# Performance work log

Hardware: AMD Instinct MI355X
Metric: run time of the kernel (lower is better)

The kernel has to match this reference:

```python
import jax, jax.numpy as jnp
import numpy as np

EPS = 1e-8  # torch.cosine_similarity default eps


def setup_inputs() -> dict:
    key = jax.random.key(0)
    ks = jax.random.split(key, 6)
    B, U, P, H = 256, 128, 64, 768
    utt_output = jax.random.normal(ks[0], (U, B, H), dtype=jnp.float32)
    pheno_output = jax.random.normal(ks[1], (P, B, H), dtype=jnp.float32)
    # Conv1d(in=U, out=U, kernel=P) weight: [out, in, kernel]
    w_utt = jax.random.normal(ks[2], (U, U, P), dtype=jnp.float32) / np.sqrt(U * P)
    b_utt = jax.random.normal(ks[3], (U,), dtype=jnp.float32) * 0.01
    # Conv1d(in=P, out=P, kernel=U) weight: [out, in, kernel]
    w_pheno = jax.random.normal(ks[4], (P, P, U), dtype=jnp.float32) / np.sqrt(P * U)
    b_pheno = jax.random.normal(ks[5], (P,), dtype=jnp.float32) * 0.01
    return {"utt_output": utt_output, "pheno_output": pheno_output,
            "w_utt": w_utt, "b_utt": b_utt, "w_pheno": w_pheno, "b_pheno": b_pheno}


def reference(utt_output, pheno_output, w_utt, b_utt, w_pheno, b_pheno):
    # [len, B, H] -> [B, len, H]
    u = jnp.swapaxes(utt_output, 0, 1)    # [B, U, H]
    p = jnp.swapaxes(pheno_output, 0, 1)  # [B, P, H]
    # cosine similarity matrix c[b,i,j] = <u_i, p_j> / (max(|u_i|,eps)*max(|p_j|,eps))
    un = u / jnp.maximum(jnp.linalg.norm(u, axis=-1, keepdims=True), EPS)
    pn = p / jnp.maximum(jnp.linalg.norm(p, axis=-1, keepdims=True), EPS)
    c = jnp.einsum('buh,bph->bup', un, pn)  # [B, U, P]
    # Conv1d with kernel covering the full width -> output length 1, i.e. an einsum
    row_logits = jnp.einsum('bup,oup->bo', c, w_utt) + b_utt        # [B, U]
    col_logits = jnp.einsum('bup,opu->bo', c, w_pheno) + b_pheno    # [B, P]
    row_attention = jax.nn.softmax(row_logits, axis=-1)
    col_attention = jax.nn.softmax(col_logits, axis=-1)
    return row_attention, col_attention
```

## Files before the change

### kernel.cpp

```cpp
#include <hip/hip_runtime.h>
#include <stdint.h>

#define Bn 256
#define Un 128
#define Pn 64
#define Hn 768
#define Ototal 192
#define KC 16

#define CH 64
#define NCH 12
#define LDU 72
#define LDB 56

typedef short s4v __attribute__((ext_vector_type(4)));
typedef short s8v __attribute__((ext_vector_type(8)));
typedef float f4v __attribute__((ext_vector_type(4)));

__device__ __forceinline__ short f2bf(float x) {
  union { float f; uint32_t u; } c; c.f = x;
  uint32_t r = (c.u + 0x7fffu + ((c.u >> 16) & 1u)) >> 16;
  return (short)(r & 0xffffu);
}

__global__ void __launch_bounds__(256) convW(const float* __restrict__ w_utt,
                                             const float* __restrict__ w_ph,
                                             ushort* __restrict__ Wbf) {
  __shared__ float tile[64 * 129];
  const int bx = blockIdx.x;
  const int t = threadIdx.x;
  if (bx < 4096) {
    int idx = bx * 256 + t;
    Wbf[idx] = (ushort)f2bf(w_utt[idx]);
    return;
  }
  const int oc = bx - 4096;
  const float* src = w_ph + (size_t)oc * 8192;
#pragma unroll
  for (int itr = 0; itr < 8; ++itr) {
    int idx = itr * 1024 + t * 4;
    int j = idx >> 7, i = idx & 127;
    float4 v = *(const float4*)(src + idx);
    tile[j * 129 + i + 0] = v.x;
    tile[j * 129 + i + 1] = v.y;
    tile[j * 129 + i + 2] = v.z;
    tile[j * 129 + i + 3] = v.w;
  }
  __syncthreads();
  const size_t obase = (size_t)(128 + oc) * 8192;
#pragma unroll
  for (int itr = 0; itr < 8; ++itr) {
    int k = itr * 1024 + t * 4;
    int i = k >> 6, j = k & 63;
    s4v o4 = { f2bf(tile[(j + 0) * 129 + i]),
               f2bf(tile[(j + 1) * 129 + i]),
               f2bf(tile[(j + 2) * 129 + i]),
               f2bf(tile[(j + 3) * 129 + i]) };
    *(s4v*)&Wbf[obase + k] = o4;
  }
}

__global__ void __launch_bounds__(1024, 4) phaseA(const float* __restrict__ utt,
                                                  const float* __restrict__ ph,
                                                  ushort* __restrict__ Cbf) {
  const int b = blockIdx.x;
  const int t = threadIdx.x;
  const int w = t >> 6, l = t & 63;

  __shared__ short uA[2][Un * LDU];
  __shared__ short pB[2][Pn * LDU];
  __shared__ float s_inu[Un];
  __shared__ float s_inp[Pn];

  const int ur = t >> 3;
  const int uc = (t & 7) * 8;
  const int pr = t >> 4;
  const int pc = (t & 15) * 4;

  const size_t rstride = (size_t)Bn * Hn;
  const float* ubase = utt + (size_t)b * Hn + (size_t)ur * rstride + uc;
  const float* pbase = ph  + (size_t)b * Hn + (size_t)pr * rstride + pc;

  float4 ru0[2], ru1[2], rp[2];
#pragma unroll
  for (int s = 0; s < 2; ++s) {
    ru0[s] = *(const float4*)(ubase + s * CH);
    ru1[s] = *(const float4*)(ubase + s * CH + 4);
    rp[s]  = *(const float4*)(pbase + s * CH);
  }

  float ssu = 0.f, ssp = 0.f;
  f4v zero4 = {0.f, 0.f, 0.f, 0.f};
  f4v acc[2] = {zero4, zero4};

  const int m  = l & 15;
  const int ko = (l >> 4) * 8;
  const int it = w & 7;
  const int jp = w >> 3;

  const int ua_w = ur * LDU + uc;
  const int pb_w = pr * LDU + pc;

#pragma unroll
  for (int c = 0; c < NCH; ++c) {
    const int s = c & 1;
    float4 a0 = ru0[s], a1 = ru1[s], p0 = rp[s];
    ssu += a0.x*a0.x + a0.y*a0.y + a0.z*a0.z + a0.w*a0.w
         + a1.x*a1.x + a1.y*a1.y + a1.z*a1.z + a1.w*a1.w;
    ssp += p0.x*p0.x + p0.y*p0.y + p0.z*p0.z + p0.w*p0.w;
    if (c + 2 < NCH) {
      ru0[s] = *(const float4*)(ubase + (c + 2) * CH);
      ru1[s] = *(const float4*)(ubase + (c + 2) * CH + 4);
      rp[s]  = *(const float4*)(pbase + (c + 2) * CH);
    }
    s8v au = { f2bf(a0.x), f2bf(a0.y), f2bf(a0.z), f2bf(a0.w),
               f2bf(a1.x), f2bf(a1.y), f2bf(a1.z), f2bf(a1.w) };
    s4v pp = { f2bf(p0.x), f2bf(p0.y), f2bf(p0.z), f2bf(p0.w) };
    *(s8v*)&uA[s][ua_w] = au;
    *(s4v*)&pB[s][pb_w] = pp;
    __syncthreads();
    const short* ab = &uA[s][(it * 16 + m) * LDU + ko];
    const short* bb = &pB[s][(jp * 32 + m) * LDU + ko];
#pragma unroll
    for (int ks = 0; ks < 2; ++ks) {
      s8v af = *(const s8v*)(ab + ks * 32);
#pragma unroll
      for (int jt = 0; jt < 2; ++jt) {
        s8v bf = *(const s8v*)(bb + jt * 16 * LDU + ks * 32);
        acc[jt] = __builtin_amdgcn_mfma_f32_16x16x32_bf16(af, bf, acc[jt], 0, 0, 0);
      }
    }
  }

  ssu += __shfl_xor(ssu, 4); ssu += __shfl_xor(ssu, 2); ssu += __shfl_xor(ssu, 1);
  ssp += __shfl_xor(ssp, 8); ssp += __shfl_xor(ssp, 4);
  ssp += __shfl_xor(ssp, 2); ssp += __shfl_xor(ssp, 1);
  if ((t & 7) == 0)  s_inu[ur] = 1.f / fmaxf(sqrtf(ssu), 1e-8f);
  if ((t & 15) == 0) s_inp[pr] = 1.f / fmaxf(sqrtf(ssp), 1e-8f);
  __syncthreads();

  const int cl = l & 15;
  const int rq = (l >> 4) * 4;
#pragma unroll
  for (int jt = 0; jt < 2; ++jt) {
    int j = jp * 32 + jt * 16 + cl;
    float sj = s_inp[j];
#pragma unroll
    for (int r = 0; r < 4; ++r) {
      int il = it * 16 + rq + r;
      float v = acc[jt][r] * s_inu[il] * sj;
      Cbf[((size_t)b * Un + il) * Pn + j] = (ushort)f2bf(v);
    }
  }
}

__global__ void __launch_bounds__(256) phaseB(const ushort* __restrict__ Cbf,
                                              const ushort* __restrict__ Wbf,
                                              float* __restrict__ partial) {
  const int kc = blockIdx.x;
  const int mt = blockIdx.y;
  const int nt = blockIdx.z;
  const int t = threadIdx.x;
  const int w = t >> 6, l = t & 63;

  __shared__ short Ab[64 * LDB];
  __shared__ short Bb[64 * LDB];

  const int row = t >> 2;
  const int ko8 = (t & 3) * 8;

  f4v zero4 = {0.f, 0.f, 0.f, 0.f};
  f4v acc[4] = {zero4, zero4, zero4, zero4};

  const ushort* Ag = Cbf + (size_t)(mt * 64 + row) * 8192 + kc * 512 + ko8;
  const ushort* Bg = Wbf + (size_t)(nt * 64 + row) * 8192 + kc * 512 + ko8;
  const int m  = l & 15;
  const int ko = (l >> 4) * 8;

  for (int c = 0; c < 16; ++c) {
    s8v av = *(const s8v*)(Ag + c * 32);
    s8v bv = *(const s8v*)(Bg + c * 32);
    __syncthreads();
    *(s8v*)&Ab[row * LDB + ko8] = av;
    *(s8v*)&Bb[row * LDB + ko8] = bv;
    __syncthreads();
    s8v af = *(const s8v*)&Ab[(16 * w + m) * LDB + ko];
#pragma unroll
    for (int jt = 0; jt < 4; ++jt) {
      s8v bf = *(const s8v*)&Bb[(16 * jt + m) * LDB + ko];
      acc[jt] = __builtin_amdgcn_mfma_f32_16x16x32_bf16(af, bf, acc[jt], 0, 0, 0);
    }
  }

  const int rq = (l >> 4) * 4;
#pragma unroll
  for (int jt = 0; jt < 4; ++jt) {
    int og = nt * 64 + 16 * jt + (l & 15);
#pragma unroll
    for (int r = 0; r < 4; ++r) {
      int bg = mt * 64 + 16 * w + rq + r;
      partial[((size_t)kc * Bn + bg) * Ototal + og] = acc[jt][r];
    }
  }
}

__global__ void __launch_bounds__(192) phaseC(const float* __restrict__ partial,
                                              const float* __restrict__ b_utt,
                                              const float* __restrict__ b_ph,
                                              float* __restrict__ out) {
  const int b = blockIdx.x;
  const int t = threadIdx.x;
  const int w = t >> 6, l = t & 63;

  float v = 0.f;
#pragma unroll
  for (int kc = 0; kc < KC; ++kc)
    v += partial[((size_t)kc * Bn + b) * Ototal + t];
  v += (t < Un) ? b_utt[t] : b_ph[t - Un];

  __shared__ float red[3];
  float mx = v;
  for (int o = 32; o >= 1; o >>= 1) mx = fmaxf(mx, __shfl_xor(mx, o));
  if (l == 0) red[w] = mx;
  __syncthreads();
  float gmax = (t < Un) ? fmaxf(red[0], red[1]) : red[2];
  float e = expf(v - gmax);
  float s = e;
  for (int o = 32; o >= 1; o >>= 1) s += __shfl_xor(s, o);
  __syncthreads();
  if (l == 0) red[w] = s;
  __syncthreads();
  float gs = (t < Un) ? (red[0] + red[1]) : red[2];
  float r = e / gs;
  if (t < Un) out[(size_t)b * Un + t] = r;
  else        out[(size_t)Bn * Un + (size_t)b * Pn + (t - Un)] = r;
}

extern "C" void kernel_launch(void* const* d_in, const int* in_sizes, int n_in,
                              void* d_out, int out_size, void* d_ws, size_t ws_size,
                              hipStream_t stream) {
  const float* utt   = (const float*)d_in[0];
  const float* ph    = (const float*)d_in[1];
  const float* w_utt = (const float*)d_in[2];
  const float* b_utt = (const float*)d_in[3];
  const float* w_ph  = (const float*)d_in[4];
  const float* b_ph  = (const float*)d_in[5];

  char* ws = (char*)d_ws;
  ushort* Cbf     = (ushort*)(ws);
  ushort* Wbf     = (ushort*)(ws + 4194304);
  float*  partial = (float*)(ws + 7340032);

  convW <<<dim3(4096 + 64), dim3(256), 0, stream>>>(w_utt, w_ph, Wbf);
  phaseA<<<dim3(Bn), dim3(1024), 0, stream>>>(utt, ph, Cbf);
  phaseB<<<dim3(KC, 4, 3), dim3(256), 0, stream>>>(Cbf, Wbf, partial);
  phaseC<<<dim3(Bn), dim3(192), 0, stream>>>(partial, b_utt, b_ph, (float*)d_out);
}
```

Baseline: 245.7 us.

## Split phaseA per batch into two U-halves and widen phaseB K-step

phaseA now launches two 512-thread blocks per batch, each computing the cosine block for 64 of the 128 utterance rows. The H loop moves to 32-wide chunks with single-buffered shared memory and a one-step register prefetch. The change is meant to raise block count and occupancy and to shrink per-block shared memory, at the cost of the pheno rows being loaded and normalised twice. phaseB now stages 64 K-values per barrier pair instead of 32, which halves its synchronisations and issues two MFMA k-steps per stage.

```diff
diff --git a/kernel.cpp b/kernel.cpp
--- a/kernel.cpp
+++ b/kernel.cpp
@@ -8,10 +8,8 @@
 #define Ototal 192
 #define KC 16
 
-#define CH 64
-#define NCH 12
-#define LDU 72
-#define LDB 56
+#define LDU 40
+#define LDB 72
 
 typedef short s4v __attribute__((ext_vector_type(4)));
 typedef short s8v __attribute__((ext_vector_type(8)));
@@ -60,83 +58,69 @@
   }
 }
 
-__global__ void __launch_bounds__(1024, 4) phaseA(const float* __restrict__ utt,
-                                                  const float* __restrict__ ph,
-                                                  ushort* __restrict__ Cbf) {
-  const int b = blockIdx.x;
+__global__ void __launch_bounds__(512) phaseA(const float* __restrict__ utt,
+                                              const float* __restrict__ ph,
+                                              ushort* __restrict__ Cbf) {
+  const int bx = blockIdx.x;
+  const int b = bx >> 1, half = bx & 1;
   const int t = threadIdx.x;
   const int w = t >> 6, l = t & 63;
 
-  __shared__ short uA[2][Un * LDU];
-  __shared__ short pB[2][Pn * LDU];
-  __shared__ float s_inu[Un];
-  __shared__ float s_inp[Pn];
-
-  const int ur = t >> 3;
-  const int uc = (t & 7) * 8;
-  const int pr = t >> 4;
-  const int pc = (t & 15) * 4;
+  __shared__ short uA[64 * LDU];
+  __shared__ short pB[64 * LDU];
+  __shared__ float s_inu[64];
+  __shared__ float s_inp[64];
+
+  const int r  = t >> 3;
+  const int cc = (t & 7) * 4;
 
   const size_t rstride = (size_t)Bn * Hn;
-  const float* ubase = utt + (size_t)b * Hn + (size_t)ur * rstride + uc;
-  const float* pbase = ph  + (size_t)b * Hn + (size_t)pr * rstride + pc;
-
-  float4 ru0[2], ru1[2], rp[2];
-#pragma unroll
-  for (int s = 0; s < 2; ++s) {
-    ru0[s] = *(const float4*)(ubase + s * CH);
-    ru1[s] = *(const float4*)(ubase + s * CH + 4);
-    rp[s]  = *(const float4*)(pbase + s * CH);
-  }
+  const float* ubase = utt + (size_t)b * Hn + (size_t)(half * 64 + r) * rstride + cc;
+  const float* pbase = ph  + (size_t)b * Hn + (size_t)r * rstride + cc;
+
+  float4 ru = *(const float4*)ubase;
+  float4 rp = *(const float4*)pbase;
 
   float ssu = 0.f, ssp = 0.f;
   f4v zero4 = {0.f, 0.f, 0.f, 0.f};
-  f4v acc[2] = {zero4, zero4};
+  f4v acc0 = zero4, acc1 = zero4;
 
   const int m  = l & 15;
   const int ko = (l >> 4) * 8;
-  const int it = w & 7;
-  const int jp = w >> 3;
-
-  const int ua_w = ur * LDU + uc;
-  const int pb_w = pr * LDU + pc;
-
-#pragma unroll
-  for (int c = 0; c < NCH; ++c) {
-    const int s = c & 1;
-    float4 a0 = ru0[s], a1 = ru1[s], p0 = rp[s];
-    ssu += a0.x*a0.x + a0.y*a0.y + a0.z*a0.z + a0.w*a0.w
-         + a1.x*a1.x + a1.y*a1.y + a1.z*a1.z + a1.w*a1.w;
+  const int it = w & 3;
+  const int jp = w >> 2;
+  const int lw = r * LDU + (t & 7) * 4;
+
+  const short* ab = &uA[(it * 16 + m) * LDU + ko];
+  const short* bb = &pB[(jp * 32 + m) * LDU + ko];
+
+  for (int c = 0; c < 24; ++c) {
+    __syncthreads();
+    float4 a = ru, p0 = rp;
+    ssu += a.x*a.x + a.y*a.y + a.z*a.z + a.w*a.w;
     ssp += p0.x*p0.x + p0.y*p0.y + p0.z*p0.z + p0.w*p0.w;
-    if (c + 2 < NCH) {
-      ru0[s] = *(const float4*)(ubase + (c + 2) * CH);
-      ru1[s] = *(const float4*)(ubase + (c + 2) * CH + 4);
-      rp[s]  = *(const float4*)(pbase + (c + 2) * CH);
-    }
-    s8v au = { f2bf(a0.x), f2bf(a0.y), f2bf(a0.z), f2bf(a0.w),
-               f2bf(a1.x), f2bf(a1.y), f2bf(a1.z), f2bf(a1.w) };
+    s4v au = { f2bf(a.x),  f2bf(a.y),  f2bf(a.z),  f2bf(a.w)  };
     s4v pp = { f2bf(p0.x), f2bf(p0.y), f2bf(p0.z), f2bf(p0.w) };
-    *(s8v*)&uA[s][ua_w] = au;
-    *(s4v*)&pB[s][pb_w] = pp;
-    __syncthreads();
-    const short* ab = &uA[s][(it * 16 + m) * LDU + ko];
-    const short* bb = &pB[s][(jp * 32 + m) * LDU + ko];
-#pragma unroll
-    for (int ks = 0; ks < 2; ++ks) {
-      s8v af = *(const s8v*)(ab + ks * 32);
-#pragma unroll
-      for (int jt = 0; jt < 2; ++jt) {
-        s8v bf = *(const s8v*)(bb + jt * 16 * LDU + ks * 32);
-        acc[jt] = __builtin_amdgcn_mfma_f32_16x16x32_bf16(af, bf, acc[jt], 0, 0, 0);
-      }
-    }
+    *(s4v*)&uA[lw] = au;
+    *(s4v*)&pB[lw] = pp;
+    __syncthreads();
+    if (c < 23) {
+      ru = *(const float4*)(ubase + (c + 1) * 32);
+      rp = *(const float4*)(pbase + (c + 1) * 32);
+    }
+    s8v af  = *(const s8v*)ab;
+    s8v bf0 = *(const s8v*)bb;
+    s8v bf1 = *(const s8v*)(bb + 16 * LDU);
+    acc0 = __builtin_amdgcn_mfma_f32_16x16x32_bf16(af, bf0, acc0, 0, 0, 0);
+    acc1 = __builtin_amdgcn_mfma_f32_16x16x32_bf16(af, bf1, acc1, 0, 0, 0);
   }
 
   ssu += __shfl_xor(ssu, 4); ssu += __shfl_xor(ssu, 2); ssu += __shfl_xor(ssu, 1);
-  ssp += __shfl_xor(ssp, 8); ssp += __shfl_xor(ssp, 4);
-  ssp += __shfl_xor(ssp, 2); ssp += __shfl_xor(ssp, 1);
-  if ((t & 7) == 0)  s_inu[ur] = 1.f / fmaxf(sqrtf(ssu), 1e-8f);
-  if ((t & 15) == 0) s_inp[pr] = 1.f / fmaxf(sqrtf(ssp), 1e-8f);
+  ssp += __shfl_xor(ssp, 4); ssp += __shfl_xor(ssp, 2); ssp += __shfl_xor(ssp, 1);
+  if ((t & 7) == 0) {
+    s_inu[r] = 1.f / fmaxf(sqrtf(ssu), 1e-8f);
+    s_inp[r] = 1.f / fmaxf(sqrtf(ssp), 1e-8f);
+  }
   __syncthreads();
 
   const int cl = l & 15;
@@ -145,11 +129,12 @@
   for (int jt = 0; jt < 2; ++jt) {
     int j = jp * 32 + jt * 16 + cl;
     float sj = s_inp[j];
-#pragma unroll
-    for (int r = 0; r < 4; ++r) {
-      int il = it * 16 + rq + r;
-      float v = acc[jt][r] * s_inu[il] * sj;
-      Cbf[((size_t)b * Un + il) * Pn + j] = (ushort)f2bf(v);
+    f4v a = (jt == 0) ? acc0 : acc1;
+#pragma unroll
+    for (int rr = 0; rr < 4; ++rr) {
+      int il = it * 16 + rq + rr;
+      float v = a[rr] * s_inu[il] * sj;
+      Cbf[((size_t)b * Un + half * 64 + il) * Pn + j] = (ushort)f2bf(v);
     }
   }
 }
@@ -167,28 +152,35 @@
   __shared__ short Bb[64 * LDB];
 
   const int row = t >> 2;
-  const int ko8 = (t & 3) * 8;
+  const int k16 = (t & 3) * 16;
 
   f4v zero4 = {0.f, 0.f, 0.f, 0.f};
   f4v acc[4] = {zero4, zero4, zero4, zero4};
 
-  const ushort* Ag = Cbf + (size_t)(mt * 64 + row) * 8192 + kc * 512 + ko8;
-  const ushort* Bg = Wbf + (size_t)(nt * 64 + row) * 8192 + kc * 512 + ko8;
+  const ushort* Ag = Cbf + (size_t)(mt * 64 + row) * 8192 + kc * 512 + k16;
+  const ushort* Bg = Wbf + (size_t)(nt * 64 + row) * 8192 + kc * 512 + k16;
   const int m  = l & 15;
   const int ko = (l >> 4) * 8;
 
-  for (int c = 0; c < 16; ++c) {
-    s8v av = *(const s8v*)(Ag + c * 32);
-    s8v bv = *(const s8v*)(Bg + c * 32);
-    __syncthreads();
-    *(s8v*)&Ab[row * LDB + ko8] = av;
-    *(s8v*)&Bb[row * LDB + ko8] = bv;
-    __syncthreads();
-    s8v af = *(const s8v*)&Ab[(16 * w + m) * LDB + ko];
-#pragma unroll
-    for (int jt = 0; jt < 4; ++jt) {
-      s8v bf = *(const s8v*)&Bb[(16 * jt + m) * LDB + ko];
-      acc[jt] = __builtin_amdgcn_mfma_f32_16x16x32_bf16(af, bf, acc[jt], 0, 0, 0);
+  for (int c = 0; c < 8; ++c) {
+    s8v av0 = *(const s8v*)(Ag + c * 64);
+    s8v av1 = *(const s8v*)(Ag + c * 64 + 8);
+    s8v bv0 = *(const s8v*)(Bg + c * 64);
+    s8v bv1 = *(const s8v*)(Bg + c * 64 + 8);
+    __syncthreads();
+    *(s8v*)&Ab[row * LDB + k16]     = av0;
+    *(s8v*)&Ab[row * LDB + k16 + 8] = av1;
+    *(s8v*)&Bb[row * LDB + k16]     = bv0;
+    *(s8v*)&Bb[row * LDB + k16 + 8] = bv1;
+    __syncthreads();
+#pragma unroll
+    for (int ks = 0; ks < 2; ++ks) {
+      s8v af = *(const s8v*)&Ab[(16 * w + m) * LDB + ks * 32 + ko];
+#pragma unroll
+      for (int jt = 0; jt < 4; ++jt) {
+        s8v bf = *(const s8v*)&Bb[(16 * jt + m) * LDB + ks * 32 + ko];
+        acc[jt] = __builtin_amdgcn_mfma_f32_16x16x32_bf16(af, bf, acc[jt], 0, 0, 0);
+      }
     }
   }
 
@@ -252,7 +244,7 @@
   float*  partial = (float*)(ws + 7340032);
 
   convW <<<dim3(4096 + 64), dim3(256), 0, stream>>>(w_utt, w_ph, Wbf);
-  phaseA<<<dim3(Bn), dim3(1024), 0, stream>>>(utt, ph, Cbf);
+  phaseA<<<dim3(2 * Bn), dim3(512), 0, stream>>>(utt, ph, Cbf);
   phaseB<<<dim3(KC, 4, 3), dim3(256), 0, stream>>>(Cbf, Wbf, partial);
   phaseC<<<dim3(Bn), dim3(192), 0, stream>>>(partial, b_utt, b_ph, (float*)d_out);
 }
```

Result: faster. 213.2 us, median of 2 (-13.2%).
